# Performance work log

Measured on AMD Instinct MI355X. Metric: run time of the kernel, lower is better.

Reference implementation:

```python
import jax, jax.numpy as jnp
import numpy as np

E = 64   # embed_dim
H = 64   # hidden_dim
U = 16384  # num users
T = 50   # max sequence length
NI = 100000  # num_items


def setup_inputs() -> dict:
    key = jax.random.key(0)
    k1, k2, k3, k4, k5, k6, k7 = jax.random.split(key, 7)
    sequences = jax.random.randint(k1, (U, T), 0, NI, dtype=jnp.int64 if jax.config.jax_enable_x64 else jnp.int32)
    lengths = jax.random.randint(k2, (U,), 1, T + 1, dtype=sequences.dtype)
    graph_embeddings = jax.random.normal(k3, (NI, E), dtype=jnp.float32)
    s = 1.0 / np.sqrt(H)
    W_ih = jax.random.uniform(k4, (4 * H, E), minval=-s, maxval=s, dtype=jnp.float32)
    W_hh = jax.random.uniform(k5, (4 * H, H), minval=-s, maxval=s, dtype=jnp.float32)
    b_ih = jax.random.uniform(k6, (4 * H,), minval=-s, maxval=s, dtype=jnp.float32)
    b_hh = jax.random.uniform(k7, (4 * H,), minval=-s, maxval=s, dtype=jnp.float32)
    return {"sequences": sequences, "lengths": lengths, "graph_embeddings": graph_embeddings,
            "W_ih": W_ih, "W_hh": W_hh, "b_ih": b_ih, "b_hh": b_hh, "num_items": NI}


def _lstm(x, W_ih, W_hh, b_ih, b_hh):
    # x: [B, T, E] -> outputs [B, T, H]; PyTorch gate order i, f, g, o
    B = x.shape[0]
    bias = b_ih + b_hh

    def step(carry, x_t):
        h, c = carry
        gates = x_t @ W_ih.T + h @ W_hh.T + bias  # [B, 4H]
        i, f, g, o = jnp.split(gates, 4, axis=-1)
        i = jax.nn.sigmoid(i)
        f = jax.nn.sigmoid(f)
        g = jnp.tanh(g)
        o = jax.nn.sigmoid(o)
        c = f * c + i * g
        h = o * jnp.tanh(c)
        return (h, c), h

    h0 = jnp.zeros((B, H), dtype=x.dtype)
    c0 = jnp.zeros((B, H), dtype=x.dtype)
    _, hs = jax.lax.scan(step, (h0, c0), jnp.swapaxes(x, 0, 1))  # [T, B, H]
    return jnp.swapaxes(hs, 0, 1)


def reference(sequences, lengths, graph_embeddings, W_ih, W_hh, b_ih, b_hh, num_items):
    x = graph_embeddings[sequences]            # [U, T, E] gather
    outs = _lstm(x, W_ih, W_hh, b_ih, b_hh)    # [U, T, H]
    valid = (jnp.arange(T)[None, :] < lengths[:, None]).astype(outs.dtype)  # [U, T]
    flat_ids = sequences.reshape(-1)
    flat_h = (outs * valid[:, :, None]).reshape(-1, H)
    sums = jax.ops.segment_sum(flat_h, flat_ids, num_segments=num_items)    # [NI, H]
    counts = jax.ops.segment_sum(valid.reshape(-1), flat_ids, num_segments=num_items)  # [NI]
    return jnp.where(counts[:, None] > 0, sums / jnp.maximum(counts[:, None], 1.0), 0.0)
```

## Files before the change

### kernel.cpp

```cpp
#include <hip/hip_runtime.h>

#define EDIM 64
#define HDIM 64
#define S_SIG  (-1.4426950408889634f)
#define S_TANH ( 2.8853900817779268f)

typedef short bf16x8 __attribute__((ext_vector_type(8)));
typedef float f32x4  __attribute__((ext_vector_type(4)));

__device__ __forceinline__ float rcp_(float x){ return __builtin_amdgcn_rcpf(x); }
__device__ __forceinline__ float exp2_(float x){ return __builtin_amdgcn_exp2f(x); }
__device__ __forceinline__ unsigned short f2bf(float f) {
    unsigned int u = __float_as_uint(f);
    return (unsigned short)((u + 0x7FFF + ((u >> 16) & 1)) >> 16);
}
__device__ __forceinline__ bf16x8 pack8s(float4 a, float4 b, float s) {
    bf16x8 w;
    w[0]=(short)f2bf(a.x*s); w[1]=(short)f2bf(a.y*s); w[2]=(short)f2bf(a.z*s); w[3]=(short)f2bf(a.w*s);
    w[4]=(short)f2bf(b.x*s); w[5]=(short)f2bf(b.y*s); w[6]=(short)f2bf(b.z*s); w[7]=(short)f2bf(b.w*s);
    return w;
}
__device__ __forceinline__ unsigned int cvtpk(float lo, float hi) {
    unsigned int r;
    asm("v_cvt_pk_bf16_f32 %0, %1, %2" : "=v"(r) : "v"(lo), "v"(hi));
    return r;
}
__device__ __forceinline__ int hu_of(int hb, int q, int r) {
    return ((hb >> 1) << 5) + (q << 3) + ((hb & 1) << 2) + r;
}

__global__ __launch_bounds__(1024) void k_sort(const int* __restrict__ lens, int U,
                                               int* __restrict__ order) {
    __shared__ int hist[52];
    __shared__ int base[52];
    const int tid = threadIdx.x;
    if (tid < 52) hist[tid] = 0;
    __syncthreads();
    for (int u = tid; u < U; u += 1024) atomicAdd(&hist[lens[u]], 1);
    __syncthreads();
    if (tid == 0) { int s = 0; for (int l = 50; l >= 0; --l) { base[l] = s; s += hist[l]; } }
    __syncthreads();
    for (int u = tid; u < U; u += 1024) { int p = atomicAdd(&base[lens[u]], 1); order[p] = u; }
}

__global__ __launch_bounds__(256, 1) void lstm_wave(
    const int* __restrict__ seq, const int* __restrict__ lens,
    const float* __restrict__ emb,
    const float* __restrict__ W_ih, const float* __restrict__ W_hh,
    const float* __restrict__ b_ih, const float* __restrict__ b_hh,
    const int* __restrict__ order,
    float* __restrict__ out_sum, float* __restrict__ cnt,
    int U, int T)
{
    __shared__ __align__(16) unsigned char lds[4 * 4096];
    const int tid  = threadIdx.x;
    const int wv   = tid >> 6;
    const int lane = tid & 63;
    const int su   = lane & 15;
    const int q    = lane >> 4;

    bf16x8 wx[4][4][2], wh[4][4][2];
    f32x4  biasv[4][4];
    #pragma unroll
    for (int g = 0; g < 4; ++g) {
        const float s = (g == 2) ? S_TANH : S_SIG;
        #pragma unroll
        for (int hb = 0; hb < 4; ++hb) {
            const int grow = g * 64 + hu_of(hb, su >> 2, su & 3);
            const float* wi = W_ih + (size_t)grow * EDIM + q * 8;
            const float* wp = W_hh + (size_t)grow * HDIM + q * 8;
            #pragma unroll
            for (int kp = 0; kp < 2; ++kp) {
                float4 a = *reinterpret_cast<const float4*>(wi + kp * 32);
                float4 b = *reinterpret_cast<const float4*>(wi + kp * 32 + 4);
                wx[g][hb][kp] = pack8s(a, b, s);
                float4 c2 = *reinterpret_cast<const float4*>(wp + kp * 32);
                float4 d2 = *reinterpret_cast<const float4*>(wp + kp * 32 + 4);
                wh[g][hb][kp] = pack8s(c2, d2, s);
            }
            #pragma unroll
            for (int r = 0; r < 4; ++r) {
                const int gi2 = g * 64 + hu_of(hb, q, r);
                biasv[g][hb][r] = s * (b_ih[gi2] + b_hh[gi2]);
            }
        }
    }

    const int nblk = gridDim.x;
    const int grp  = (wv & 1) ? ((wv + 1) * nblk - 1 - blockIdx.x)
                              : (wv * nblk + blockIdx.x);
    const int wbase = grp * 16;
    int us = 0, len = 0;
    if (wbase + su < U) { us = order[wbase + su]; len = lens[us]; }
    const int* sp = seq + (size_t)us * T;
    int mT = len;
    mT = max(mT, __shfl_xor(mT, 1, 64));
    mT = max(mT, __shfl_xor(mT, 2, 64));
    mT = max(mT, __shfl_xor(mT, 4, 64));
    mT = max(mT, __shfl_xor(mT, 8, 64));
    if (mT <= 0) return;

    const float4* e4 = reinterpret_cast<const float4*>(emb);
    int itc = sp[0];
    int itn = (1 < mT) ? sp[1] : itc;
    bf16x8 bx0, bx1, bh0 = {0,0,0,0,0,0,0,0}, bh1 = {0,0,0,0,0,0,0,0};
    {
        const size_t eb = (size_t)itc * 16 + q * 2;
        bx0 = pack8s(e4[eb],     e4[eb + 1], 1.0f);
        bx1 = pack8s(e4[eb + 8], e4[eb + 9], 1.0f);
    }
    f32x4 cst[4] = {{0,0,0,0},{0,0,0,0},{0,0,0,0},{0,0,0,0}};
    f32x4 hs[4];
    int   itp = 0, vprev = 0;
    const int XP = wv * 4096;

    auto scatter_prev = [&]() {
        #pragma unroll
        for (int hb = 0; hb < 4; ++hb) {
            int byte = (su * 64 + hu_of(hb, q, 0)) * 4;
            byte ^= (su & 7) << 4;
            *reinterpret_cast<f32x4*>(lds + XP + byte) = hs[hb];
        }
        asm volatile("s_waitcnt lgkmcnt(0)" ::: "memory");
        #pragma unroll
        for (int g = 0; g < 16; ++g) {
            const int itg = __builtin_amdgcn_readlane(itp, g);
            const int byte = ((g * 64 + lane) * 4) ^ ((g & 7) << 4);
            const float hv = *reinterpret_cast<const float*>(lds + XP + byte);
            atomicAdd(&out_sum[(size_t)itg * HDIM + lane], hv);
        }
        if (q == 0 && vprev) atomicAdd(&cnt[itp], 1.0f);
    };

    for (int t = 0; t < mT; ++t) {
        float4 na, nb, nc, nd; int sn = itn;
        const bool pf = (t + 1 < mT);
        if (pf) {
            const size_t eb = (size_t)itn * 16 + q * 2;
            na = e4[eb]; nb = e4[eb + 1]; nc = e4[eb + 8]; nd = e4[eb + 9];
        }
        if (t + 2 < mT) sn = sp[t + 2];

        if (t > 0) scatter_prev();

        f32x4 hn[4];
        #pragma unroll
        for (int hb = 0; hb < 4; ++hb) {
            f32x4 acc[4];
            #pragma unroll
            for (int g = 0; g < 4; ++g) {
                acc[g] = biasv[g][hb];
                acc[g] = __builtin_amdgcn_mfma_f32_16x16x32_bf16(wx[g][hb][0], bx0, acc[g], 0, 0, 0);
                acc[g] = __builtin_amdgcn_mfma_f32_16x16x32_bf16(wx[g][hb][1], bx1, acc[g], 0, 0, 0);
                acc[g] = __builtin_amdgcn_mfma_f32_16x16x32_bf16(wh[g][hb][0], bh0, acc[g], 0, 0, 0);
                acc[g] = __builtin_amdgcn_mfma_f32_16x16x32_bf16(wh[g][hb][1], bh1, acc[g], 0, 0, 0);
            }
            #pragma unroll
            for (int r = 0; r < 4; ++r) {
                const float ei = exp2_(acc[0][r]);
                const float ef = exp2_(acc[1][r]);
                const float eg = exp2_(acc[2][r]);
                const float eo = exp2_(acc[3][r]);
                const float gi = rcp_(1.0f + ei);
                const float gf = rcp_(1.0f + ef);
                const float gg = 1.0f - 2.0f * rcp_(1.0f + eg);
                const float go = rcp_(1.0f + eo);
                const float cc = gf * cst[hb][r] + gi * gg;
                cst[hb][r] = cc;
                const float et = exp2_(S_TANH * cc);
                const float th = 1.0f - 2.0f * rcp_(1.0f + et);
                hn[hb][r] = go * th;
            }
        }
        uint4 p0, p1;
        p0.x = cvtpk(hn[0][0], hn[0][1]); p0.y = cvtpk(hn[0][2], hn[0][3]);
        p0.z = cvtpk(hn[1][0], hn[1][1]); p0.w = cvtpk(hn[1][2], hn[1][3]);
        p1.x = cvtpk(hn[2][0], hn[2][1]); p1.y = cvtpk(hn[2][2], hn[2][3]);
        p1.z = cvtpk(hn[3][0], hn[3][1]); p1.w = cvtpk(hn[3][2], hn[3][3]);
        bh0 = __builtin_bit_cast(bf16x8, p0);
        bh1 = __builtin_bit_cast(bf16x8, p1);

        const int val = (t < len) ? 1 : 0;
        const float vm = val ? 1.0f : 0.0f;
        #pragma unroll
        for (int hb = 0; hb < 4; ++hb)
            #pragma unroll
            for (int r = 0; r < 4; ++r) hs[hb][r] = hn[hb][r] * vm;
        itp = itc; vprev = val;

        if (pf) { bx0 = pack8s(na, nb, 1.0f); bx1 = pack8s(nc, nd, 1.0f); itc = itn; itn = sn; }
    }
    scatter_prev();
}

__global__ __launch_bounds__(256) void finalize_mean(
    float* __restrict__ out, const float* __restrict__ cnt, int NI)
{
    const int idx = blockIdx.x * blockDim.x + threadIdx.x;
    const int total = NI * (HDIM / 4);
    if (idx >= total) return;
    const int i = idx >> 4;
    const float c = cnt[i];
    const float s = (c > 0.0f) ? __builtin_amdgcn_rcpf(c) : 0.0f;
    float4* o = reinterpret_cast<float4*>(out);
    float4 v = o[idx];
    v.x *= s; v.y *= s; v.z *= s; v.w *= s;
    o[idx] = v;
}

extern "C" void kernel_launch(void* const* d_in, const int* in_sizes, int n_in,
                              void* d_out, int out_size, void* d_ws, size_t ws_size,
                              hipStream_t stream)
{
    const int*   seq  = (const int*)d_in[0];
    const int*   lens = (const int*)d_in[1];
    const float* emb  = (const float*)d_in[2];
    const float* W_ih = (const float*)d_in[3];
    const float* W_hh = (const float*)d_in[4];
    const float* b_ih = (const float*)d_in[5];
    const float* b_hh = (const float*)d_in[6];
    float* out = (float*)d_out;

    const int U  = in_sizes[1];
    const int T  = in_sizes[0] / U;
    const int NI = in_sizes[2] / EDIM;

    float* cnt   = (float*)d_ws;
    int*   order = (int*)d_ws + NI;

    hipMemsetAsync(out, 0, (size_t)NI * HDIM * sizeof(float), stream);
    hipMemsetAsync(cnt, 0, (size_t)NI * sizeof(float), stream);

    k_sort<<<1, 1024, 0, stream>>>(lens, U, order);

    const int nblk = (U + 63) / 64;
    lstm_wave<<<nblk, 256, 0, stream>>>(seq, lens, emb, W_ih, W_hh, b_ih, b_hh,
                                        order, out, cnt, U, T);

    const int total = NI * (HDIM / 4);
    finalize_mean<<<(total + 255) / 256, 256, 0, stream>>>(out, cnt, NI);
}
```

Measured before the change: 299.4 us.

## Move W_ih fragments to LDS, halve users per wave, double occupancy

```diff
diff --git a/kernel.cpp b/kernel.cpp
--- a/kernel.cpp
+++ b/kernel.cpp
@@ -4,6 +4,7 @@
 #define HDIM 64
 #define S_SIG  (-1.4426950408889634f)
 #define S_TANH ( 2.8853900817779268f)
+#define UPW 8
 
 typedef short bf16x8 __attribute__((ext_vector_type(8)));
 typedef float f32x4  __attribute__((ext_vector_type(4)));
@@ -31,19 +32,30 @@
 
 __global__ __launch_bounds__(1024) void k_sort(const int* __restrict__ lens, int U,
                                                int* __restrict__ order) {
-    __shared__ int hist[52];
+    __shared__ int whist[16][52];
     __shared__ int base[52];
     const int tid = threadIdx.x;
-    if (tid < 52) hist[tid] = 0;
-    __syncthreads();
-    for (int u = tid; u < U; u += 1024) atomicAdd(&hist[lens[u]], 1);
-    __syncthreads();
-    if (tid == 0) { int s = 0; for (int l = 50; l >= 0; --l) { base[l] = s; s += hist[l]; } }
+    const int w = tid >> 6, l = tid & 63;
+    for (int i = l; i < 52; i += 64) whist[w][i] = 0;
+    __syncthreads();
+    for (int u = tid; u < U; u += 1024) atomicAdd(&whist[w][lens[u]], 1);
+    __syncthreads();
+    if (tid < 52) {
+        int s = 0;
+        #pragma unroll
+        for (int ww = 0; ww < 16; ++ww) s += whist[ww][tid];
+        base[tid] = s;
+    }
+    __syncthreads();
+    if (tid == 0) {
+        int s = 0;
+        for (int b = 51; b >= 0; --b) { int c = base[b]; base[b] = s; s += c; }
+    }
     __syncthreads();
     for (int u = tid; u < U; u += 1024) { int p = atomicAdd(&base[lens[u]], 1); order[p] = u; }
 }
 
-__global__ __launch_bounds__(256, 1) void lstm_wave(
+__global__ __launch_bounds__(256, 2) void lstm_wave(
     const int* __restrict__ seq, const int* __restrict__ lens,
     const float* __restrict__ emb,
     const float* __restrict__ W_ih, const float* __restrict__ W_hh,
@@ -52,46 +64,55 @@
     float* __restrict__ out_sum, float* __restrict__ cnt,
     int U, int T)
 {
-    __shared__ __align__(16) unsigned char lds[4 * 4096];
+    __shared__ __align__(16) unsigned char lds[32768 + 16384];
     const int tid  = threadIdx.x;
     const int wv   = tid >> 6;
     const int lane = tid & 63;
     const int su   = lane & 15;
     const int q    = lane >> 4;
 
-    bf16x8 wx[4][4][2], wh[4][4][2];
+    for (int s = tid; s < 2048; s += 256) {
+        const int rt = s >> 7, kt = (s >> 6) & 1, l = s & 63;
+        const int g = rt >> 2, hb = rt & 3;
+        const int rho = l & 15, qf = l >> 4;
+        const float sg = (g == 2) ? S_TANH : S_SIG;
+        const int grow = g * 64 + hu_of(hb, rho >> 2, rho & 3);
+        const float* src = W_ih + (size_t)grow * EDIM + kt * 32 + qf * 8;
+        float4 a = *reinterpret_cast<const float4*>(src);
+        float4 b = *reinterpret_cast<const float4*>(src + 4);
+        *reinterpret_cast<bf16x8*>(lds + (size_t)s * 16) = pack8s(a, b, sg);
+    }
+
+    bf16x8 wh[4][4][2];
     f32x4  biasv[4][4];
     #pragma unroll
     for (int g = 0; g < 4; ++g) {
-        const float s = (g == 2) ? S_TANH : S_SIG;
+        const float sg = (g == 2) ? S_TANH : S_SIG;
         #pragma unroll
         for (int hb = 0; hb < 4; ++hb) {
             const int grow = g * 64 + hu_of(hb, su >> 2, su & 3);
-            const float* wi = W_ih + (size_t)grow * EDIM + q * 8;
             const float* wp = W_hh + (size_t)grow * HDIM + q * 8;
             #pragma unroll
             for (int kp = 0; kp < 2; ++kp) {
-                float4 a = *reinterpret_cast<const float4*>(wi + kp * 32);
-                float4 b = *reinterpret_cast<const float4*>(wi + kp * 32 + 4);
-                wx[g][hb][kp] = pack8s(a, b, s);
                 float4 c2 = *reinterpret_cast<const float4*>(wp + kp * 32);
                 float4 d2 = *reinterpret_cast<const float4*>(wp + kp * 32 + 4);
-                wh[g][hb][kp] = pack8s(c2, d2, s);
+                wh[g][hb][kp] = pack8s(c2, d2, sg);
             }
             #pragma unroll
             for (int r = 0; r < 4; ++r) {
                 const int gi2 = g * 64 + hu_of(hb, q, r);
-                biasv[g][hb][r] = s * (b_ih[gi2] + b_hh[gi2]);
-            }
-        }
-    }
+                biasv[g][hb][r] = sg * (b_ih[gi2] + b_hh[gi2]);
+            }
+        }
+    }
+    __syncthreads();
 
     const int nblk = gridDim.x;
     const int grp  = (wv & 1) ? ((wv + 1) * nblk - 1 - blockIdx.x)
                               : (wv * nblk + blockIdx.x);
-    const int wbase = grp * 16;
+    const int wbase = grp * UPW;
     int us = 0, len = 0;
-    if (wbase + su < U) { us = order[wbase + su]; len = lens[us]; }
+    if (su < UPW && wbase + su < U) { us = order[wbase + su]; len = lens[us]; }
     const int* sp = seq + (size_t)us * T;
     int mT = len;
     mT = max(mT, __shfl_xor(mT, 1, 64));
@@ -112,7 +133,7 @@
     f32x4 cst[4] = {{0,0,0,0},{0,0,0,0},{0,0,0,0},{0,0,0,0}};
     f32x4 hs[4];
     int   itp = 0, vprev = 0;
-    const int XP = wv * 4096;
+    const int XP = 32768 + wv * 4096;
 
     auto scatter_prev = [&]() {
         #pragma unroll
@@ -123,7 +144,7 @@
         }
         asm volatile("s_waitcnt lgkmcnt(0)" ::: "memory");
         #pragma unroll
-        for (int g = 0; g < 16; ++g) {
+        for (int g = 0; g < UPW; ++g) {
             const int itg = __builtin_amdgcn_readlane(itp, g);
             const int byte = ((g * 64 + lane) * 4) ^ ((g & 7) << 4);
             const float hv = *reinterpret_cast<const float*>(lds + XP + byte);
@@ -146,29 +167,31 @@
         f32x4 hn[4];
         #pragma unroll
         for (int hb = 0; hb < 4; ++hb) {
+            bf16x8 wx0[4], wx1[4];
+            #pragma unroll
+            for (int g = 0; g < 4; ++g) {
+                const int rt = g * 4 + hb;
+                wx0[g] = *reinterpret_cast<const bf16x8*>(lds + ((rt * 2 + 0) * 64 + lane) * 16);
+                wx1[g] = *reinterpret_cast<const bf16x8*>(lds + ((rt * 2 + 1) * 64 + lane) * 16);
+            }
             f32x4 acc[4];
             #pragma unroll
             for (int g = 0; g < 4; ++g) {
                 acc[g] = biasv[g][hb];
-                acc[g] = __builtin_amdgcn_mfma_f32_16x16x32_bf16(wx[g][hb][0], bx0, acc[g], 0, 0, 0);
-                acc[g] = __builtin_amdgcn_mfma_f32_16x16x32_bf16(wx[g][hb][1], bx1, acc[g], 0, 0, 0);
+                acc[g] = __builtin_amdgcn_mfma_f32_16x16x32_bf16(wx0[g], bx0, acc[g], 0, 0, 0);
+                acc[g] = __builtin_amdgcn_mfma_f32_16x16x32_bf16(wx1[g], bx1, acc[g], 0, 0, 0);
                 acc[g] = __builtin_amdgcn_mfma_f32_16x16x32_bf16(wh[g][hb][0], bh0, acc[g], 0, 0, 0);
                 acc[g] = __builtin_amdgcn_mfma_f32_16x16x32_bf16(wh[g][hb][1], bh1, acc[g], 0, 0, 0);
             }
             #pragma unroll
             for (int r = 0; r < 4; ++r) {
-                const float ei = exp2_(acc[0][r]);
-                const float ef = exp2_(acc[1][r]);
-                const float eg = exp2_(acc[2][r]);
-                const float eo = exp2_(acc[3][r]);
-                const float gi = rcp_(1.0f + ei);
-                const float gf = rcp_(1.0f + ef);
-                const float gg = 1.0f - 2.0f * rcp_(1.0f + eg);
-                const float go = rcp_(1.0f + eo);
+                const float gi = rcp_(1.0f + exp2_(acc[0][r]));
+                const float gf = rcp_(1.0f + exp2_(acc[1][r]));
+                const float gg = 1.0f - 2.0f * rcp_(1.0f + exp2_(acc[2][r]));
+                const float go = rcp_(1.0f + exp2_(acc[3][r]));
                 const float cc = gf * cst[hb][r] + gi * gg;
                 cst[hb][r] = cc;
-                const float et = exp2_(S_TANH * cc);
-                const float th = 1.0f - 2.0f * rcp_(1.0f + et);
+                const float th = 1.0f - 2.0f * rcp_(1.0f + exp2_(S_TANH * cc));
                 hn[hb][r] = go * th;
             }
         }
@@ -233,7 +256,7 @@
 
     k_sort<<<1, 1024, 0, stream>>>(lens, U, order);
 
-    const int nblk = (U + 63) / 64;
+    const int nblk = (U + 4 * UPW - 1) / (4 * UPW);
     lstm_wave<<<nblk, 256, 0, stream>>>(seq, lens, emb, W_ih, W_hh, b_ih, b_hh,
                                         order, out, cnt, U, T);
 
```

New measurement: 480.2 us. +60.4%, slower.
